# Optimization experiments

Hardware: AMD Instinct MI355X
Metric: run time of the kernel (lower is better)

The kernel has to match this reference:

```python
import jax, jax.numpy as jnp
import numpy as np
import math

BS, SL, NE, NH = 4, 2048, 1024, 16
HD = NE // NH  # 64


def setup_inputs() -> dict:
    key = jax.random.key(0)
    ks = jax.random.split(key, 5)
    x = jax.random.normal(ks[0], (BS, SL, NE), dtype=jnp.float32)
    # causal mask: 1 where attending allowed (j <= i), 0 otherwise
    mask = jnp.tril(jnp.ones((SL, SL), dtype=jnp.int32))[None, None, :, :]
    s = 1.0 / math.sqrt(NE)
    Wqkv = jax.random.normal(ks[1], (NE, 3 * NE), dtype=jnp.float32) * s
    bqkv = jax.random.normal(ks[2], (3 * NE,), dtype=jnp.float32) * 0.02
    Wo = jax.random.normal(ks[3], (NE, NE), dtype=jnp.float32) * s
    bo = jax.random.normal(ks[4], (NE,), dtype=jnp.float32) * 0.02
    return {"x": x, "mask": mask, "Wqkv": Wqkv, "bqkv": bqkv, "Wo": Wo, "bo": bo}


def reference(x, mask, Wqkv, bqkv, Wo, bo):
    bs, sl, ne = x.shape
    qkv = x @ Wqkv + bqkv                       # [bs, sl, 3*ne]
    q, k, v = jnp.split(qkv, 3, axis=-1)
    # [bs, sl, ne] -> [bs, nh, sl, hd]
    q = q.reshape(bs, sl, NH, HD).transpose(0, 2, 1, 3)
    k = k.reshape(bs, sl, NH, HD).transpose(0, 2, 1, 3)
    v = v.reshape(bs, sl, NH, HD).transpose(0, 2, 1, 3)
    scale = 1.0 / math.sqrt(HD)
    att = jnp.einsum('bhqd,bhkd->bhqk', q, k) * scale  # [bs, nh, sl, sl]
    att = jnp.where(mask == 0, -jnp.inf, att)
    w = jax.nn.softmax(att, axis=-1)
    y = jnp.einsum('bhqk,bhkd->bhqd', w, v)            # [bs, nh, sl, hd]
    y = y.transpose(0, 2, 1, 3).reshape(bs, sl, ne)
    return y @ Wo + bo
```

## Files before the change

### kernel.cpp

```cpp
#include <hip/hip_runtime.h>

#define BS 4
#define SL 2048
#define NE 1024
#define NH 16
#define HD 64
#define N3 3072

typedef __attribute__((ext_vector_type(8))) __bf16 bf16x8;
typedef __attribute__((ext_vector_type(4))) float f32x4;
typedef __attribute__((ext_vector_type(4))) short s16x4;
typedef unsigned short u16;

__device__ __forceinline__ u16 f2bf(float f) {
  union { float f; unsigned int u; } v; v.f = f;
  unsigned int r = v.u + 0x7FFFu + ((v.u >> 16) & 1u);
  return (u16)(r >> 16);
}
__device__ __forceinline__ int pack_bf2(float a, float b) {
  union { float f; unsigned int u; } x, y; x.f = a; y.f = b;
  return (int)((y.u & 0xFFFF0000u) | (x.u >> 16));
}

__device__ __forceinline__ void gld16(const void* g, void* l) {
#if __has_builtin(__builtin_amdgcn_global_load_lds)
  __builtin_amdgcn_global_load_lds(
      (const __attribute__((address_space(1))) unsigned int*)g,
      (__attribute__((address_space(3))) unsigned int*)l, 16, 0, 0);
#else
  *(int4*)((char*)l + (size_t)(threadIdx.x & 63) * 16) = *(const int4*)g;
#endif
}

__global__ void convert_x(const float* __restrict__ x, u16* __restrict__ xb) {
  int i = (blockIdx.x * 256 + threadIdx.x) * 8;
  float4 f0 = *(const float4*)(x + i);
  float4 f1 = *(const float4*)(x + i + 4);
  union { int4 v; u16 h[8]; } p;
  p.h[0] = f2bf(f0.x); p.h[1] = f2bf(f0.y);
  p.h[2] = f2bf(f0.z); p.h[3] = f2bf(f0.w);
  p.h[4] = f2bf(f1.x); p.h[5] = f2bf(f1.y);
  p.h[6] = f2bf(f1.z); p.h[7] = f2bf(f1.w);
  *(int4*)(xb + i) = p.v;
}

__global__ void transpose_w(const float* __restrict__ W, u16* __restrict__ Wt,
                            int K, int N) {
  __shared__ u16 tile[32][33];
  int bn = blockIdx.x * 32, bk = blockIdx.y * 32;
  int tx = threadIdx.x, ty = threadIdx.y;
  for (int r = 0; r < 32; r += 8)
    tile[ty + r][tx] = f2bf(W[(size_t)(bk + ty + r) * N + bn + tx]);
  __syncthreads();
  for (int r = 0; r < 32; r += 8)
    Wt[(size_t)(bn + ty + r) * K + bk + tx] = tile[tx][ty + r];
}

template <int C32>
__global__ __launch_bounds__(256) void gemm_bt(
    const u16* __restrict__ A, const u16* __restrict__ Bt,
    const float* __restrict__ bias, void* __restrict__ C, int M, int N, int K,
    int lda) {
  __shared__ u16 As[128 * 32];
  __shared__ u16 Bs[128 * 32];

  const int tid = threadIdx.x;
  const int wave = tid >> 6, lane = tid & 63;
  const int lq = lane >> 4, lr = lane & 15;
  const int m0 = blockIdx.y * 128, n0 = blockIdx.x * 128;
  const int wm = (wave & 1) * 64, wn = (wave >> 1) * 64;

  const f32x4 fzero = {0.f, 0.f, 0.f, 0.f};
  f32x4 acc[4][4];
#pragma unroll
  for (int i = 0; i < 4; i++)
#pragma unroll
    for (int j = 0; j < 4; j++) acc[i][j] = fzero;

  for (int k0 = 0; k0 < K; k0 += 32) {
    __syncthreads();
#pragma unroll
    for (int t = 0; t < 2; t++) {
      int chunk = wave * 2 + t;
      const u16* ga = A + (size_t)(m0 + chunk * 16 + (lane >> 2)) * lda + k0 +
                      (lane & 3) * 8;
      gld16(ga, &As[chunk * 512]);
      const u16* gb = Bt + (size_t)(n0 + chunk * 16 + (lane >> 2)) * K + k0 +
                      (lane & 3) * 8;
      gld16(gb, &Bs[chunk * 512]);
    }
    __syncthreads();

    bf16x8 af[4], bfr[4];
#pragma unroll
    for (int i = 0; i < 4; i++)
      af[i] = *(const bf16x8*)&As[(wm + i * 16 + lr) * 32 + lq * 8];
#pragma unroll
    for (int j = 0; j < 4; j++)
      bfr[j] = *(const bf16x8*)&Bs[(wn + j * 16 + lr) * 32 + lq * 8];
#pragma unroll
    for (int i = 0; i < 4; i++)
#pragma unroll
      for (int j = 0; j < 4; j++)
        acc[i][j] = __builtin_amdgcn_mfma_f32_16x16x32_bf16(af[i], bfr[j],
                                                            acc[i][j], 0, 0, 0);
  }

#pragma unroll
  for (int j = 0; j < 4; j++) {
    int col = n0 + wn + j * 16 + lr;
    float bv = bias[col];
#pragma unroll
    for (int i = 0; i < 4; i++) {
#pragma unroll
      for (int r = 0; r < 4; r++) {
        int row = m0 + wm + i * 16 + lq * 4 + r;
        float val = acc[i][j][r] + bv;
        if (C32) ((float*)C)[(size_t)row * N + col] = val;
        else     ((u16*)C)[(size_t)row * N + col]   = f2bf(val);
      }
    }
  }
}

#define KSTR 72
#define MFMA16(a, b, c) __builtin_amdgcn_mfma_f32_16x16x32_bf16(a, b, c, 0, 0, 0)
#define MFMA1616(a, b, c) \
  __builtin_amdgcn_mfma_f32_16x16x16bf16_1k(a, b, c, 0, 0, 0)

__device__ __forceinline__ void attn_step(const bf16x8& q0, const bf16x8& q1,
                                          const u16* __restrict__ Kb,
                                          const u16* __restrict__ Vs,
                                          bool diag, int w, int lq, int lr,
                                          f32x4 (&o)[4], float& m_, float& l_) {
  const f32x4 fzero = {0.f, 0.f, 0.f, 0.f};
  const int swz = (lq ^ (lr & 3)) * 8;
  f32x4 s[4];
  __builtin_amdgcn_s_setprio(1);
#pragma unroll
  for (int j = 0; j < 4; j++) {
    int kr = j * 16 + lr;
    bf16x8 kf0 = *(const bf16x8*)&Kb[kr * 32 + swz];
    bf16x8 kf1 = *(const bf16x8*)&Kb[2048 + kr * 32 + swz];
    f32x4 z = MFMA16(kf0, q0, fzero);
    s[j] = MFMA16(kf1, q1, z);
  }
  __builtin_amdgcn_s_setprio(0);
  if (diag) {
    int qloc = w * 16 + lr - 4 * lq;
#pragma unroll
    for (int j = 0; j < 4; j++)
#pragma unroll
      for (int r = 0; r < 4; r++)
        if (16 * j + r > qloc) s[j][r] = -1e30f;
  }
  float mt = s[0][0];
#pragma unroll
  for (int j = 0; j < 4; j++)
#pragma unroll
    for (int r = 0; r < 4; r++) mt = fmaxf(mt, s[j][r]);
  mt = fmaxf(mt, __shfl_xor(mt, 16));
  mt = fmaxf(mt, __shfl_xor(mt, 32));
  float mn = m_;
  if (!__all(mt <= m_ + 64.0f)) {
    mn = fmaxf(m_, mt);
    float alpha = __expf((m_ - mn) * 0.125f);
    m_ = mn;
    l_ *= alpha;
#pragma unroll
    for (int jd = 0; jd < 4; jd++)
#pragma unroll
      for (int r = 0; r < 4; r++) o[jd][r] *= alpha;
  }
  s16x4 pa[4];
  float psum = 0.f;
#pragma unroll
  for (int j = 0; j < 4; j++) {
    float p0 = __expf((s[j][0] - mn) * 0.125f);
    float p1 = __expf((s[j][1] - mn) * 0.125f);
    float p2 = __expf((s[j][2] - mn) * 0.125f);
    float p3 = __expf((s[j][3] - mn) * 0.125f);
    psum += (p0 + p1) + (p2 + p3);
    union { int i[2]; s16x4 v; } pu;
    pu.i[0] = pack_bf2(p0, p1);
    pu.i[1] = pack_bf2(p2, p3);
    pa[j] = pu.v;
  }
  l_ += psum;
  __builtin_amdgcn_s_setprio(1);
#pragma unroll
  for (int jd = 0; jd < 4; jd++) {
    const u16* vrow = &Vs[(jd * 16 + lr) * KSTR + lq * 16];
    union { int4 q; s16x4 h[2]; } va, vb;
    va.q = *(const int4*)vrow;
    vb.q = *(const int4*)(vrow + 8);
    o[jd] = MFMA1616(va.h[0], pa[0], o[jd]);
    o[jd] = MFMA1616(va.h[1], pa[1], o[jd]);
    o[jd] = MFMA1616(vb.h[0], pa[2], o[jd]);
    o[jd] = MFMA1616(vb.h[1], pa[3], o[jd]);
  }
  __builtin_amdgcn_s_setprio(0);
}

__global__ __launch_bounds__(256, 4) void attn_paired(u16* __restrict__ qkv) {
  __shared__ u16 Ks[2][4096];
  __shared__ u16 Vs[64 * KSTR];

  const int tid = threadIdx.x;
  const int w = tid >> 6, lane = tid & 63;
  const int lq = lane >> 4, lr = lane & 15;
  const int bh = blockIdx.x, p = blockIdx.y;
  const int h = bh & (NH - 1), b = bh >> 4;
  const int qt0 = p, qt1 = (SL / 64 - 1) - p;

  u16* base = qkv + (size_t)b * SL * N3;
  const u16* kbase = base + NE + h * HD;

  const int kg_key = lane >> 2;
  const int kg_blk = (lane & 3) ^ (kg_key & 3);
  const int skey = tid & 63, sd0 = (tid >> 6) * 8;
  const int skeyP = ((skey >> 2) & 3) * 16 + (skey >> 4) * 4 + (skey & 3);
  const u16* vrow0 = base + (size_t)skey * N3 + 2 * NE + h * HD + sd0;

#define KPRE(buf, key0)                                                     \
  {                                                                         \
    _Pragma("unroll") for (int t = 0; t < 2; t++) {                         \
      int chunk = w * 2 + t, half = chunk >> 2, kgrp = chunk & 3;           \
      const u16* g = kbase + (size_t)((key0) + kgrp * 16 + kg_key) * N3 +   \
                     half * 32 + kg_blk * 8;                                \
      gld16(g, &Ks[buf][half * 2048 + kgrp * 512]);                         \
    }                                                                       \
  }

  bf16x8 qf[2][2];
#pragma unroll
  for (int half = 0; half < 2; half++) {
    int qt = half ? qt1 : qt0;
    const u16* qrow = base + (size_t)(qt * 64 + w * 16 + lr) * N3 + h * HD;
    qf[half][0] = *(const bf16x8*)(qrow + lq * 8);
    qf[half][1] = *(const bf16x8*)(qrow + 32 + lq * 8);
  }

  const f32x4 fzero = {0.f, 0.f, 0.f, 0.f};
  f32x4 o[2][4];
  float m_[2], l_[2];
#pragma unroll
  for (int half = 0; half < 2; half++) {
    m_[half] = -1e30f;
    l_[half] = 0.f;
#pragma unroll
    for (int jd = 0; jd < 4; jd++) o[half][jd] = fzero;
  }

  KPRE(0, 0);
  int4 v0 = *(const int4*)vrow0;
  int4 v1 = *(const int4*)(vrow0 + 32);

  const int ktend = qt1 + 1;
  for (int kt = 0; kt < ktend; kt++) {
    __syncthreads();
    {
      union { int4 v; u16 u[8]; } t0, t1;
      t0.v = v0; t1.v = v1;
#pragma unroll
      for (int j = 0; j < 8; j++) {
        Vs[(sd0 + j) * KSTR + skeyP] = t0.u[j];
        Vs[(sd0 + 32 + j) * KSTR + skeyP] = t1.u[j];
      }
    }
    __syncthreads();

    if (kt + 1 < ktend) {
      KPRE((kt + 1) & 1, (kt + 1) * 64);
      const u16* nv = vrow0 + (size_t)(kt + 1) * 64 * N3;
      v0 = *(const int4*)nv;
      v1 = *(const int4*)(nv + 32);
    }

    const u16* Kb = &Ks[kt & 1][0];
    attn_step(qf[1][0], qf[1][1], Kb, Vs, kt == qt1, w, lq, lr, o[1], m_[1],
              l_[1]);
    if (kt <= qt0)
      attn_step(qf[0][0], qf[0][1], Kb, Vs, kt == qt0, w, lq, lr, o[0], m_[0],
                l_[0]);
  }

#pragma unroll
  for (int half = 0; half < 2; half++) {
    int qt = half ? qt1 : qt0;
    float lsum = l_[half];
    lsum += __shfl_xor(lsum, 16);
    lsum += __shfl_xor(lsum, 32);
    float inv = 1.0f / lsum;
    u16* yrow = base + (size_t)(qt * 64 + w * 16 + lr) * N3 + h * HD;
#pragma unroll
    for (int jd = 0; jd < 4; jd++) {
      int2 val;
      val.x = (int)(((unsigned)f2bf(o[half][jd][1] * inv) << 16) |
                    f2bf(o[half][jd][0] * inv));
      val.y = (int)(((unsigned)f2bf(o[half][jd][3] * inv) << 16) |
                    f2bf(o[half][jd][2] * inv));
      *(int2*)(yrow + 16 * jd + 4 * lq) = val;
    }
  }
}

extern "C" void kernel_launch(void* const* d_in, const int* in_sizes, int n_in,
                              void* d_out, int out_size, void* d_ws,
                              size_t ws_size, hipStream_t stream) {
  const float* x    = (const float*)d_in[0];
  const float* Wqkv = (const float*)d_in[2];
  const float* bqkv = (const float*)d_in[3];
  const float* Wo   = (const float*)d_in[4];
  const float* bo   = (const float*)d_in[5];

  u16* WqkvT  = (u16*)d_ws;
  u16* WoT    = WqkvT + (size_t)N3 * NE;
  u16* xb     = WoT + (size_t)NE * NE;
  u16* qkvbuf = xb + (size_t)BS * SL * NE;

  convert_x<<<(BS * SL * NE) / (256 * 8), 256, 0, stream>>>(x, xb);
  transpose_w<<<dim3(N3 / 32, NE / 32), dim3(32, 8), 0, stream>>>(Wqkv, WqkvT,
                                                                  NE, N3);
  transpose_w<<<dim3(NE / 32, NE / 32), dim3(32, 8), 0, stream>>>(Wo, WoT, NE,
                                                                  NE);
  gemm_bt<0><<<dim3(N3 / 128, (BS * SL) / 128), 256, 0, stream>>>(
      xb, WqkvT, bqkv, qkvbuf, BS * SL, N3, NE, NE);
  attn_paired<<<dim3(BS * NH, SL / 128), 256, 0, stream>>>(qkvbuf);
  gemm_bt<1><<<dim3(NE / 128, (BS * SL) / 128), 256, 0, stream>>>(
      qkvbuf, WoT, bo, d_out, BS * SL, NE, NE, N3);
}
```

Before: 283.3 us.

## Replace GEMM with 256-row tiled, double-buffered 8-wave pipelined kernel

```diff
diff --git a/kernel.cpp b/kernel.cpp
--- a/kernel.cpp
+++ b/kernel.cpp
@@ -56,71 +56,152 @@
     Wt[(size_t)(bn + ty + r) * K + bk + tx] = tile[tx][ty + r];
 }
 
-template <int C32>
-__global__ __launch_bounds__(256) void gemm_bt(
+#define VMW(n) asm volatile("s_waitcnt vmcnt(" #n ")" ::: "memory")
+#define BARR()                         \
+  do {                                 \
+    __builtin_amdgcn_s_barrier();      \
+    __builtin_amdgcn_sched_barrier(0); \
+  } while (0)
+#define MFMA_G(a, b, c) \
+  __builtin_amdgcn_mfma_f32_16x16x32_bf16(a, b, c, 0, 0, 0)
+
+template <int C32, int BN>
+__global__ __launch_bounds__(512, 2) void gemm8p(
     const u16* __restrict__ A, const u16* __restrict__ Bt,
     const float* __restrict__ bias, void* __restrict__ C, int M, int N, int K,
     int lda) {
-  __shared__ u16 As[128 * 32];
-  __shared__ u16 Bs[128 * 32];
+  constexpr int BM = 256, BK = 64;
+  constexpr int NF = BN / 64;
+  constexpr int NHALF = NF / 2;
+  __shared__ u16 As[2][BM * BK];
+  __shared__ u16 Bs[2][BN * BK];
 
   const int tid = threadIdx.x;
-  const int wave = tid >> 6, lane = tid & 63;
+  const int w = tid >> 6, lane = tid & 63;
   const int lq = lane >> 4, lr = lane & 15;
-  const int m0 = blockIdx.y * 128, n0 = blockIdx.x * 128;
-  const int wm = (wave & 1) * 64, wn = (wave >> 1) * 64;
+  const int m0 = blockIdx.y * BM, n0 = blockIdx.x * BN;
+
+  const int l8 = lane >> 3, lb = lane & 7;
+  const int swz8 = ((lb ^ l8) * 8);
+  const u16* gA = A + (size_t)(m0 + w * 16 + l8) * lda + swz8;
+  const u16* gB =
+      (BN == 256) ? Bt + (size_t)(n0 + w * 16 + l8) * K + swz8
+                  : Bt + (size_t)(n0 + w * 8 + l8) * K + swz8;
+
+#define STAGE_A(buf, half, gp)                                        \
+  do {                                                                \
+    gld16((gp) + (size_t)((half) * 128) * lda,                        \
+          &As[buf][(half) * 8192 + (2 * w) * 512]);                   \
+    gld16((gp) + (size_t)((half) * 128 + 8) * lda,                    \
+          &As[buf][(half) * 8192 + (2 * w + 1) * 512]);               \
+  } while (0)
+#define STAGE_B(buf, half, gp)                                        \
+  do {                                                                \
+    if constexpr (BN == 256) {                                        \
+      gld16((gp) + (size_t)((half) * 128) * K,                        \
+            &Bs[buf][(half) * 8192 + (2 * w) * 512]);                 \
+      gld16((gp) + (size_t)((half) * 128 + 8) * K,                    \
+            &Bs[buf][(half) * 8192 + (2 * w + 1) * 512]);             \
+    } else {                                                          \
+      gld16((gp) + (size_t)((half) * 64) * K,                         \
+            &Bs[buf][(half) * 4096 + w * 512]);                       \
+    }                                                                 \
+  } while (0)
+#define READ_A(buf, half)                                                    \
+  _Pragma("unroll") for (int i = 0; i < 4; i++) _Pragma("unroll") for (       \
+      int ks = 0; ks < 2; ks++) {                                            \
+    int row = (half) * 128 + (w >> 2) * 64 + i * 16 + lr;                    \
+    a[i][ks] =                                                               \
+        *(const bf16x8*)&As[buf][row * 64 + (((ks * 4 + lq) ^ (lr & 7)) * 8)]; \
+  }
+#define READ_B(buf, nh)                                                      \
+  _Pragma("unroll") for (int jj = 0; jj < NHALF; jj++) _Pragma("unroll") for ( \
+      int ks = 0; ks < 2; ks++) {                                            \
+    int row = (BN == 256) ? ((nh) * 128 + (w & 3) * 32 + jj * 16 + lr)       \
+                          : ((nh) * 64 + (w & 3) * 16 + lr);                 \
+    bb[nh][jj][ks] =                                                         \
+        *(const bf16x8*)&Bs[buf][row * 64 + (((ks * 4 + lq) ^ (lr & 7)) * 8)]; \
+  }
+#define MFMA_PHASE(ilo, nh)                                                  \
+  do {                                                                       \
+    __builtin_amdgcn_s_setprio(1);                                          \
+    _Pragma("unroll") for (int i = 0; i < 4; i++) _Pragma("unroll") for (     \
+        int jj = 0; jj < NHALF; jj++) _Pragma("unroll") for (int ks = 0;     \
+                                                             ks < 2; ks++)   \
+        acc[(ilo) + i][(nh)*NHALF + jj] = MFMA_G(                            \
+            a[i][ks], bb[nh][jj][ks], acc[(ilo) + i][(nh)*NHALF + jj]);      \
+    __builtin_amdgcn_s_setprio(0);                                          \
+  } while (0)
 
   const f32x4 fzero = {0.f, 0.f, 0.f, 0.f};
-  f32x4 acc[4][4];
-#pragma unroll
-  for (int i = 0; i < 4; i++)
-#pragma unroll
-    for (int j = 0; j < 4; j++) acc[i][j] = fzero;
-
-  for (int k0 = 0; k0 < K; k0 += 32) {
-    __syncthreads();
-#pragma unroll
-    for (int t = 0; t < 2; t++) {
-      int chunk = wave * 2 + t;
-      const u16* ga = A + (size_t)(m0 + chunk * 16 + (lane >> 2)) * lda + k0 +
-                      (lane & 3) * 8;
-      gld16(ga, &As[chunk * 512]);
-      const u16* gb = Bt + (size_t)(n0 + chunk * 16 + (lane >> 2)) * K + k0 +
-                      (lane & 3) * 8;
-      gld16(gb, &Bs[chunk * 512]);
+  f32x4 acc[8][NF];
+#pragma unroll
+  for (int i = 0; i < 8; i++)
+#pragma unroll
+    for (int j = 0; j < NF; j++) acc[i][j] = fzero;
+
+  const int KT = K / BK;
+  STAGE_A(0, 0, gA);
+  STAGE_B(0, 0, gB);
+  STAGE_B(0, 1, gB);
+  STAGE_A(0, 1, gA);
+  const u16* gAn = gA + BK;
+  const u16* gBn = gB + BK;
+
+  for (int T = 0; T < KT; T++) {
+    const int cur = T & 1, nxt = cur ^ 1;
+    const bool pf = (T + 1 < KT);
+    bf16x8 a[4][2], bb[2][NHALF][2];
+    if (BN == 256) { VMW(4); } else { VMW(3); }
+    BARR();
+    READ_A(cur, 0);
+    READ_B(cur, 0);
+    if (pf) STAGE_A(nxt, 0, gAn);
+    MFMA_PHASE(0, 0);
+    if (pf) { VMW(4); } else { VMW(2); }
+    BARR();
+    READ_B(cur, 1);
+    if (pf) STAGE_B(nxt, 0, gBn);
+    MFMA_PHASE(0, 1);
+    if (pf) {
+      if (BN == 256) { VMW(4); } else { VMW(3); }
+    } else {
+      VMW(0);
     }
-    __syncthreads();
-
-    bf16x8 af[4], bfr[4];
-#pragma unroll
-    for (int i = 0; i < 4; i++)
-      af[i] = *(const bf16x8*)&As[(wm + i * 16 + lr) * 32 + lq * 8];
-#pragma unroll
-    for (int j = 0; j < 4; j++)
-      bfr[j] = *(const bf16x8*)&Bs[(wn + j * 16 + lr) * 32 + lq * 8];
-#pragma unroll
-    for (int i = 0; i < 4; i++)
-#pragma unroll
-      for (int j = 0; j < 4; j++)
-        acc[i][j] = __builtin_amdgcn_mfma_f32_16x16x32_bf16(af[i], bfr[j],
-                                                            acc[i][j], 0, 0, 0);
-  }
-
-#pragma unroll
-  for (int j = 0; j < 4; j++) {
-    int col = n0 + wn + j * 16 + lr;
+    BARR();
+    READ_A(cur, 1);
+    if (pf) STAGE_B(nxt, 1, gBn);
+    MFMA_PHASE(4, 1);
+    if (pf) STAGE_A(nxt, 1, gAn);
+    MFMA_PHASE(4, 0);
+    gAn += BK;
+    gBn += BK;
+  }
+
+#pragma unroll
+  for (int j = 0; j < NF; j++) {
+    int col;
+    if (BN == 256)
+      col = n0 + (j >> 1) * 128 + (w & 3) * 32 + (j & 1) * 16 + lr;
+    else
+      col = n0 + j * 64 + (w & 3) * 16 + lr;
     float bv = bias[col];
 #pragma unroll
-    for (int i = 0; i < 4; i++) {
+    for (int i = 0; i < 8; i++) {
+      int rbase = m0 + (i >> 2) * 128 + (w >> 2) * 64 + (i & 3) * 16 + lq * 4;
 #pragma unroll
       for (int r = 0; r < 4; r++) {
-        int row = m0 + wm + i * 16 + lq * 4 + r;
         float val = acc[i][j][r] + bv;
-        if (C32) ((float*)C)[(size_t)row * N + col] = val;
-        else     ((u16*)C)[(size_t)row * N + col]   = f2bf(val);
+        if (C32) ((float*)C)[(size_t)(rbase + r) * N + col] = val;
+        else     ((u16*)C)[(size_t)(rbase + r) * N + col]   = f2bf(val);
       }
     }
   }
+#undef STAGE_A
+#undef STAGE_B
+#undef READ_A
+#undef READ_B
+#undef MFMA_PHASE
 }
 
 #define KSTR 72
@@ -324,9 +405,9 @@
                                                                   NE, N3);
   transpose_w<<<dim3(NE / 32, NE / 32), dim3(32, 8), 0, stream>>>(Wo, WoT, NE,
                                                                   NE);
-  gemm_bt<0><<<dim3(N3 / 128, (BS * SL) / 128), 256, 0, stream>>>(
+  gemm8p<0, 256><<<dim3(N3 / 256, (BS * SL) / 256), 512, 0, stream>>>(
       xb, WqkvT, bqkv, qkvbuf, BS * SL, N3, NE, NE);
   attn_paired<<<dim3(BS * NH, SL / 128), 256, 0, stream>>>(qkvbuf);
-  gemm_bt<1><<<dim3(NE / 128, (BS * SL) / 128), 256, 0, stream>>>(
+  gemm8p<1, 128><<<dim3(NE / 128, (BS * SL) / 256), 512, 0, stream>>>(
       qkvbuf, WoT, bo, d_out, BS * SL, NE, NE, N3);
 }
```

Measured after the change: 268.9 us. 5.1% less time.

## Double-buffer GEMM K-loop with BK=64, XOR-swizzled LDS and XCD-aware tile remap

Applied to the files above, without the earlier changes.

```diff
diff --git a/kernel.cpp b/kernel.cpp
--- a/kernel.cpp
+++ b/kernel.cpp
@@ -56,19 +56,43 @@
     Wt[(size_t)(bn + ty + r) * K + bk + tx] = tile[tx][ty + r];
 }
 
+#define MFMA_G(a, b, c) \
+  __builtin_amdgcn_mfma_f32_16x16x32_bf16(a, b, c, 0, 0, 0)
+
 template <int C32>
-__global__ __launch_bounds__(256) void gemm_bt(
+__global__ __launch_bounds__(256, 2) void gemm2b(
     const u16* __restrict__ A, const u16* __restrict__ Bt,
     const float* __restrict__ bias, void* __restrict__ C, int M, int N, int K,
     int lda) {
-  __shared__ u16 As[128 * 32];
-  __shared__ u16 Bs[128 * 32];
+  constexpr int BM = 128, BN = 128, BK = 64;
+  __shared__ u16 As[2][BM * BK];
+  __shared__ u16 Bs[2][BN * BK];
 
   const int tid = threadIdx.x;
-  const int wave = tid >> 6, lane = tid & 63;
+  const int w = tid >> 6, lane = tid & 63;
   const int lq = lane >> 4, lr = lane & 15;
-  const int m0 = blockIdx.y * 128, n0 = blockIdx.x * 128;
-  const int wm = (wave & 1) * 64, wn = (wave >> 1) * 64;
+  const int nwx = gridDim.x;
+  const int nwg = nwx * gridDim.y;
+  const int lin = blockIdx.y * nwx + blockIdx.x;
+  const int cpx = nwg >> 3;
+  const int swb = (lin & 7) * cpx + (lin >> 3);
+  const int m0 = (swb / nwx) * BM, n0 = (swb % nwx) * BN;
+  const int wm = (w >> 1) * 64, wn = (w & 1) * 64;
+
+  const int l8 = lane >> 3, lb = lane & 7;
+  const int sw8 = (lb ^ l8) * 8;
+  const u16* gA = A + (size_t)(m0 + w * 32 + l8) * lda + sw8;
+  const u16* gB = Bt + (size_t)(n0 + w * 32 + l8) * K + sw8;
+
+#define STAGE(buf, gpa, gpb)                                  \
+  do {                                                        \
+    _Pragma("unroll") for (int c = 0; c < 4; c++) {           \
+      gld16((gpa) + (size_t)(c * 8) * lda,                    \
+            &As[buf][(w * 32 + c * 8) * 64]);                 \
+      gld16((gpb) + (size_t)(c * 8) * K,                      \
+            &Bs[buf][(w * 32 + c * 8) * 64]);                 \
+    }                                                         \
+  } while (0)
 
   const f32x4 fzero = {0.f, 0.f, 0.f, 0.f};
   f32x4 acc[4][4];
@@ -77,34 +101,50 @@
 #pragma unroll
     for (int j = 0; j < 4; j++) acc[i][j] = fzero;
 
-  for (int k0 = 0; k0 < K; k0 += 32) {
+  const int KT = K / BK;
+  STAGE(0, gA, gB);
+  __syncthreads();
+  const u16* gAn = gA + BK;
+  const u16* gBn = gB + BK;
+
+  for (int T = 0; T < KT; T++) {
+    const int cur = T & 1;
+    if (T + 1 < KT) {
+      STAGE(cur ^ 1, gAn, gBn);
+      gAn += BK;
+      gBn += BK;
+    }
+    __builtin_amdgcn_sched_barrier(0);
+
+    bf16x8 a[4][2], bfr[4][2];
+#pragma unroll
+    for (int i = 0; i < 4; i++)
+#pragma unroll
+      for (int ks = 0; ks < 2; ks++) {
+        int row = wm + i * 16 + lr;
+        a[i][ks] = *(const bf16x8*)
+            &As[cur][row * 64 + (((ks * 4 + lq) ^ (lr & 7)) * 8)];
+      }
+#pragma unroll
+    for (int j = 0; j < 4; j++)
+#pragma unroll
+      for (int ks = 0; ks < 2; ks++) {
+        int row = wn + j * 16 + lr;
+        bfr[j][ks] = *(const bf16x8*)
+            &Bs[cur][row * 64 + (((ks * 4 + lq) ^ (lr & 7)) * 8)];
+      }
+    __builtin_amdgcn_s_setprio(1);
+#pragma unroll
+    for (int ks = 0; ks < 2; ks++)
+#pragma unroll
+      for (int i = 0; i < 4; i++)
+#pragma unroll
+        for (int j = 0; j < 4; j++)
+          acc[i][j] = MFMA_G(a[i][ks], bfr[j][ks], acc[i][j]);
+    __builtin_amdgcn_s_setprio(0);
     __syncthreads();
-#pragma unroll
-    for (int t = 0; t < 2; t++) {
-      int chunk = wave * 2 + t;
-      const u16* ga = A + (size_t)(m0 + chunk * 16 + (lane >> 2)) * lda + k0 +
-                      (lane & 3) * 8;
-      gld16(ga, &As[chunk * 512]);
-      const u16* gb = Bt + (size_t)(n0 + chunk * 16 + (lane >> 2)) * K + k0 +
-                      (lane & 3) * 8;
-      gld16(gb, &Bs[chunk * 512]);
-    }
-    __syncthreads();
-
-    bf16x8 af[4], bfr[4];
-#pragma unroll
-    for (int i = 0; i < 4; i++)
-      af[i] = *(const bf16x8*)&As[(wm + i * 16 + lr) * 32 + lq * 8];
-#pragma unroll
-    for (int j = 0; j < 4; j++)
-      bfr[j] = *(const bf16x8*)&Bs[(wn + j * 16 + lr) * 32 + lq * 8];
-#pragma unroll
-    for (int i = 0; i < 4; i++)
-#pragma unroll
-      for (int j = 0; j < 4; j++)
-        acc[i][j] = __builtin_amdgcn_mfma_f32_16x16x32_bf16(af[i], bfr[j],
-                                                            acc[i][j], 0, 0, 0);
-  }
+  }
+#undef STAGE
 
 #pragma unroll
   for (int j = 0; j < 4; j++) {
@@ -324,9 +364,9 @@
                                                                   NE, N3);
   transpose_w<<<dim3(NE / 32, NE / 32), dim3(32, 8), 0, stream>>>(Wo, WoT, NE,
                                                                   NE);
-  gemm_bt<0><<<dim3(N3 / 128, (BS * SL) / 128), 256, 0, stream>>>(
+  gemm2b<0><<<dim3(N3 / 128, (BS * SL) / 128), 256, 0, stream>>>(
       xb, WqkvT, bqkv, qkvbuf, BS * SL, N3, NE, NE);
   attn_paired<<<dim3(BS * NH, SL / 128), 256, 0, stream>>>(qkvbuf);
-  gemm_bt<1><<<dim3(NE / 128, (BS * SL) / 128), 256, 0, stream>>>(
+  gemm2b<1><<<dim3(NE / 128, (BS * SL) / 128), 256, 0, stream>>>(
       qkvbuf, WoT, bo, d_out, BS * SL, NE, NE, N3);
 }
```

Result: faster. 262.4 us (-7.4%).
